# Performance work log

Measured on AMD Instinct MI355X. Metric: run time of the kernel, lower is better.

## Reference

```python
import jax, jax.numpy as jnp
import numpy as np

# KernelConv config (pinned by hard-coded views in the source)
KS = [1, 3, 5, 7]          # sorted kernel sizes
KTOT = sum(KS)             # 16
KMAX = KS[-1]              # 7
COLOR = 4                  # packed Bayer channels
RGB = 3
H = W = 48                 # hard-coded in source view


def setup_inputs() -> dict:
    key = jax.random.key(0)
    k1, k2, k3 = jax.random.split(key, 3)
    B, N = 4, 8
    frames = jax.random.normal(k1, (B, N, COLOR, H, W), dtype=jnp.float32)
    # core channels = N * 2*KTOT * COLOR * RGB = 8 * 32 * 12 = 3072
    core = jax.random.normal(k2, (B, N * 2 * KTOT * COLOR * RGB, H, W), dtype=jnp.float32)
    kernel_weight = jax.random.uniform(k3, (B, N, len(KS), RGB, H, W), dtype=jnp.float32)
    return {"frames": frames, "core": core, "kernel_weight": kernel_weight}


def _kernel_conv(frames, core, kernel_weight):
    B, N, color, h, w = frames.shape
    # --- _sep_conv_core: separable 1D cores -> 2D per-pixel cores (outer product) ---
    c = core.reshape(B, N, 2 * KTOT, color, RGB, h, w)
    c1, c2 = c[:, :, :KTOT], c[:, :, KTOT:]
    cores = {}
    cur = 0
    for K in KS:
        t1 = c1[:, :, cur:cur + K]          # [B,N,K,color,3,h,w]
        t2 = c2[:, :, cur:cur + K]
        # outer product over the two kernel axes (torch einsum ijklcnop,ijlmcnop->ijkmcnop)
        cores[K] = jnp.einsum('bnkcthw,bnlcthw->bnklcthw', t1, t2)  # [B,N,K,K,color,3,h,w]
        cur += K
    # --- pad all kernels to KMAX and stack (reversed kernel order, as in source) ---
    padded = []
    for K in KS[::-1]:
        p = (KMAX - K) // 2
        padded.append(jnp.pad(cores[K], ((0, 0), (0, 0), (p, p), (p, p), (0, 0), (0, 0), (0, 0), (0, 0))))
    pk = jnp.stack(padded, axis=2)                              # [B,N,S,KMAX,KMAX,color,3,h,w]
    pk = pk.reshape(B, N, len(KS), KMAX * KMAX * color, RGB, h, w)
    # weighted fusion across kernel scales
    wk = jnp.mean(pk * kernel_weight[:, :, :, None], axis=2)    # [B,N,KMAX^2*color,3,h,w]
    # --- img_stack: KMAX^2 shifted views of the padded frames ---
    r = KMAX // 2
    fpad = jnp.pad(frames, ((0, 0), (0, 0), (0, 0), (r, r), (r, r)))
    shifts = [fpad[..., i:i + h, j:j + w] for i in range(KMAX) for j in range(KMAX)]
    img_stack = jnp.stack(shifts, axis=2)                       # [B,N,KMAX^2,color,h,w]
    # --- per-pixel conv: sum over kernel taps and color for each RGB output ---
    wk_r = wk.reshape(B, N, KMAX * KMAX, color, RGB, h, w)
    pred_img_i = jnp.einsum('bnkcthw,bnkchw->bnthw', wk_r, img_stack)  # [B,N,3,h,w]
    pred_img = jnp.mean(pred_img_i, axis=1)                            # [B,3,h,w]
    return pred_img_i, pred_img


def reference(frames, core, kernel_weight):
    return _kernel_conv(frames, core, kernel_weight)
```

## Files before the change

### kernel.cpp

```cpp
#include <hip/hip_runtime.h>

#define HH 48
#define WW 48
#define HW 2304
#define NB 8
#define CB 4
#define TB 3


__global__ __launch_bounds__(256) void kconv_part(
    const float* __restrict__ frames,
    const float* __restrict__ core,
    const float* __restrict__ kw,
    float* __restrict__ part)
{
    const int tid = blockIdx.x * blockDim.x + threadIdx.x;
    const int pix = tid % HW;
    int rem = tid / HW;
    const int t = rem % TB; rem /= TB;
    const int c = rem % CB; rem /= CB;
    const int n = rem % NB;
    const int b = rem / NB;
    const int x = pix % WW;
    const int y = pix / WW;

    const float* kwp = kw + ((size_t)(b * NB + n) * 12 + t) * HW + pix;
    const float kw0 = kwp[0];
    const float kw1 = kwp[(size_t)3 * HW];
    const float kw2 = kwp[(size_t)6 * HW];
    const float kw3 = kwp[(size_t)9 * HW];

    const float* cp = core + ((size_t)b * 3072 + (size_t)((n * 32) * CB + c) * 3 + t) * HW + pix;
    float a[16], bv[16];
    #pragma unroll
    for (int q = 0; q < 16; ++q) {
        a[q]  = cp[(size_t)(q * 12) * HW];
        bv[q] = cp[(size_t)((q + 16) * 12) * HW];
    }

    const float* fb = frames + ((size_t)(b * NB + n) * CB + c) * HW;

    float r7 = 0.f, r5 = 0.f, r3 = 0.f, r1 = 0.f;
    #pragma unroll
    for (int i = 0; i < 7; ++i) {
        const int yy = y + i - 3;
        const bool yok = (yy >= 0) & (yy < HH);
        float fp[7];
        #pragma unroll
        for (int j = 0; j < 7; ++j) {
            const int xx = x + j - 3;
            const bool ok = yok & (xx >= 0) & (xx < WW);
            fp[j] = ok ? fb[yy * WW + xx] : 0.f;
        }
        float in7 = 0.f;
        #pragma unroll
        for (int j = 0; j < 7; ++j) in7 = fmaf(bv[9 + j], fp[j], in7);
        r7 = fmaf(a[9 + i], in7, r7);
        if (i >= 1 && i <= 5) {
            float in5 = 0.f;
            #pragma unroll
            for (int j = 0; j < 5; ++j) in5 = fmaf(bv[4 + j], fp[1 + j], in5);
            r5 = fmaf(a[4 + i - 1], in5, r5);
        }
        if (i >= 2 && i <= 4) {
            float in3 = 0.f;
            #pragma unroll
            for (int j = 0; j < 3; ++j) in3 = fmaf(bv[1 + j], fp[2 + j], in3);
            r3 = fmaf(a[1 + i - 2], in3, r3);
        }
        if (i == 3) r1 = a[0] * bv[0] * fp[3];
    }

    part[tid] = fmaf(kw0, r7, fmaf(kw1, r5, fmaf(kw2, r3, kw3 * r1)));
}

__global__ __launch_bounds__(256) void reduce_c(
    const float* __restrict__ part, float* __restrict__ out)
{
    const int tid = blockIdx.x * blockDim.x + threadIdx.x;
    const int pix3 = tid % (TB * HW);
    const int bn = tid / (TB * HW);
    const float* p = part + (size_t)bn * CB * TB * HW + pix3;
    const float s = p[0] + p[(size_t)TB * HW] + p[(size_t)2 * TB * HW] + p[(size_t)3 * TB * HW];
    out[tid] = 0.25f * s;
}

__global__ __launch_bounds__(256) void mean_kernel(
    const float* __restrict__ pii, float* __restrict__ pm)
{
    const int tid = blockIdx.x * blockDim.x + threadIdx.x;
    if (tid >= 4 * TB * HW) return;
    const int pix3 = tid % (TB * HW);
    const int b = tid / (TB * HW);
    float s = 0.f;
    #pragma unroll
    for (int n = 0; n < NB; ++n)
        s += pii[(size_t)((b * NB + n) * TB) * HW + pix3];
    pm[tid] = s * 0.125f;
}

__global__ __launch_bounds__(256) void kconv_kernel(
    const float* __restrict__ frames, const float* __restrict__ core,
    const float* __restrict__ kw, float* __restrict__ out)
{
    const int tid = blockIdx.x * blockDim.x + threadIdx.x;
    const int x = tid % WW;
    const int y = (tid / WW) % HH;
    const int n = (tid / HW) % NB;
    const int b = tid / (HW * NB);
    const int pix = y * WW + x;

    float kwv[4][3];
    {
        const float* kwp = kw + (size_t)((b * NB + n) * 12) * HW + pix;
        #pragma unroll
        for (int s = 0; s < 4; ++s)
            #pragma unroll
            for (int t = 0; t < TB; ++t)
                kwv[s][t] = kwp[(size_t)(s * 3 + t) * HW];
    }
    float acc[TB] = {0.f, 0.f, 0.f};
    const float* fbase = frames + (size_t)((b * NB + n) * CB) * HW;
    const float* cbase = core + (size_t)b * 3072 * HW + pix;
    for (int c = 0; c < CB; ++c) {
        float fpv[49];
        #pragma unroll
        for (int i = 0; i < 7; ++i) {
            const int yy = y + i - 3;
            #pragma unroll
            for (int j = 0; j < 7; ++j) {
                const int xx = x + j - 3;
                const bool ok = (yy >= 0) & (yy < HH) & (xx >= 0) & (xx < WW);
                fpv[i * 7 + j] = ok ? fbase[(size_t)c * HW + yy * WW + xx] : 0.f;
            }
        }
        #pragma unroll
        for (int t = 0; t < TB; ++t) {
            float a[16], bv[16];
            const float* cp = cbase + (size_t)(((n * 32) * CB + c) * 3 + t) * HW;
            #pragma unroll
            for (int q = 0; q < 16; ++q) {
                a[q]  = cp[(size_t)(q * 12) * HW];
                bv[q] = cp[(size_t)((q + 16) * 12) * HW];
            }
            float tot = 0.f;
            {
                float r = 0.f;
                #pragma unroll
                for (int i = 0; i < 7; ++i) {
                    float inner = 0.f;
                    #pragma unroll
                    for (int j = 0; j < 7; ++j) inner = fmaf(bv[9 + j], fpv[i * 7 + j], inner);
                    r = fmaf(a[9 + i], inner, r);
                }
                tot = fmaf(kwv[0][t], r, tot);
            }
            {
                float r = 0.f;
                #pragma unroll
                for (int i = 0; i < 5; ++i) {
                    float inner = 0.f;
                    #pragma unroll
                    for (int j = 0; j < 5; ++j) inner = fmaf(bv[4 + j], fpv[(1 + i) * 7 + 1 + j], inner);
                    r = fmaf(a[4 + i], inner, r);
                }
                tot = fmaf(kwv[1][t], r, tot);
            }
            {
                float r = 0.f;
                #pragma unroll
                for (int i = 0; i < 3; ++i) {
                    float inner = 0.f;
                    #pragma unroll
                    for (int j = 0; j < 3; ++j) inner = fmaf(bv[1 + j], fpv[(2 + i) * 7 + 2 + j], inner);
                    r = fmaf(a[1 + i], inner, r);
                }
                tot = fmaf(kwv[2][t], r, tot);
            }
            tot = fmaf(kwv[3][t], a[0] * bv[0] * fpv[3 * 7 + 3], tot);
            acc[t] += 0.25f * tot;
        }
    }
    float* op = out + (size_t)((b * NB + n) * TB) * HW + pix;
    op[0] = acc[0]; op[HW] = acc[1]; op[2 * HW] = acc[2];
}

extern "C" void kernel_launch(void* const* d_in, const int* in_sizes, int n_in,
                              void* d_out, int out_size, void* d_ws, size_t ws_size,
                              hipStream_t stream) {
    const float* frames = (const float*)d_in[0];
    const float* core   = (const float*)d_in[1];
    const float* kw     = (const float*)d_in[2];
    float* out = (float*)d_out;
    float* pm  = out + 4 * NB * TB * HW;

    const size_t part_elems = (size_t)4 * NB * CB * TB * HW;
    if (ws_size >= part_elems * sizeof(float)) {
        float* part = (float*)d_ws;
        kconv_part<<<(int)(part_elems / 256), 256, 0, stream>>>(frames, core, kw, part);
        reduce_c<<<(4 * NB * TB * HW) / 256, 256, 0, stream>>>(part, out);
    } else {
        kconv_kernel<<<(4 * NB * HW) / 256, 256, 0, stream>>>(frames, core, kw, out);
    }
    mean_kernel<<<(4 * TB * HW + 255) / 256, 256, 0, stream>>>(out, pm);
}
```

Baseline: 30.68 us.

## Fuse channel reduction and batch mean into one finish kernel, clamp frame loads

Merges the color-channel reduction and the mean-over-frames kernels into a single finish kernel, so one launch and one round trip of the per-frame output through global memory are removed. The conv kernel now clamps frame indices and loads unconditionally before masking, which avoids divergent predicated loads. It also moves the kernel_weight loads after the compute loop and sets a minimum-occupancy hint of 6 blocks per CU. The finish kernel launches far fewer threads (one per b,t,pixel, each looping over 8 frames), so it exposes less parallelism.

```diff
diff --git a/kernel.cpp b/kernel.cpp
--- a/kernel.cpp
+++ b/kernel.cpp
@@ -8,7 +8,7 @@
 #define TB 3
 
 
-__global__ __launch_bounds__(256) void kconv_part(
+__global__ __launch_bounds__(256, 6) void kconv_part(
     const float* __restrict__ frames,
     const float* __restrict__ core,
     const float* __restrict__ kw,
@@ -24,79 +24,79 @@
     const int x = pix % WW;
     const int y = pix / WW;
 
+    const float* cp = core + ((size_t)b * 3072 + (size_t)((n * 32) * CB + c) * 3 + t) * HW + pix;
+    float a[16], bv[16];
+    #pragma unroll
+    for (int q = 0; q < 16; ++q) {
+        a[q]  = cp[(size_t)(q * 12) * HW];
+        bv[q] = cp[(size_t)((q + 16) * 12) * HW];
+    }
+
+    const float* fb = frames + ((size_t)(b * NB + n) * CB + c) * HW;
+
+    float r7 = 0.f, r5 = 0.f, r3 = 0.f, r1 = 0.f;
+    #pragma unroll
+    for (int i = 0; i < 7; ++i) {
+        const int yy = y + i - 3;
+        const bool yok = (yy >= 0) & (yy < HH);
+        const int yyc = min(max(yy, 0), HH - 1);
+        const float* frow = fb + yyc * WW;
+        float fp[7];
+        #pragma unroll
+        for (int j = 0; j < 7; ++j) {
+            const int xx = x + j - 3;
+            const bool ok = yok & (xx >= 0) & (xx < WW);
+            const int xxc = min(max(xx, 0), WW - 1);
+            const float v = frow[xxc];
+            fp[j] = ok ? v : 0.f;
+        }
+        float in7 = 0.f;
+        #pragma unroll
+        for (int j = 0; j < 7; ++j) in7 = fmaf(bv[9 + j], fp[j], in7);
+        r7 = fmaf(a[9 + i], in7, r7);
+        if (i >= 1 && i <= 5) {
+            float in5 = 0.f;
+            #pragma unroll
+            for (int j = 0; j < 5; ++j) in5 = fmaf(bv[4 + j], fp[1 + j], in5);
+            r5 = fmaf(a[4 + i - 1], in5, r5);
+        }
+        if (i >= 2 && i <= 4) {
+            float in3 = 0.f;
+            #pragma unroll
+            for (int j = 0; j < 3; ++j) in3 = fmaf(bv[1 + j], fp[2 + j], in3);
+            r3 = fmaf(a[1 + i - 2], in3, r3);
+        }
+        if (i == 3) r1 = a[0] * bv[0] * fp[3];
+    }
+
     const float* kwp = kw + ((size_t)(b * NB + n) * 12 + t) * HW + pix;
     const float kw0 = kwp[0];
     const float kw1 = kwp[(size_t)3 * HW];
     const float kw2 = kwp[(size_t)6 * HW];
     const float kw3 = kwp[(size_t)9 * HW];
 
-    const float* cp = core + ((size_t)b * 3072 + (size_t)((n * 32) * CB + c) * 3 + t) * HW + pix;
-    float a[16], bv[16];
-    #pragma unroll
-    for (int q = 0; q < 16; ++q) {
-        a[q]  = cp[(size_t)(q * 12) * HW];
-        bv[q] = cp[(size_t)((q + 16) * 12) * HW];
-    }
-
-    const float* fb = frames + ((size_t)(b * NB + n) * CB + c) * HW;
-
-    float r7 = 0.f, r5 = 0.f, r3 = 0.f, r1 = 0.f;
-    #pragma unroll
-    for (int i = 0; i < 7; ++i) {
-        const int yy = y + i - 3;
-        const bool yok = (yy >= 0) & (yy < HH);
-        float fp[7];
-        #pragma unroll
-        for (int j = 0; j < 7; ++j) {
-            const int xx = x + j - 3;
-            const bool ok = yok & (xx >= 0) & (xx < WW);
-            fp[j] = ok ? fb[yy * WW + xx] : 0.f;
-        }
-        float in7 = 0.f;
-        #pragma unroll
-        for (int j = 0; j < 7; ++j) in7 = fmaf(bv[9 + j], fp[j], in7);
-        r7 = fmaf(a[9 + i], in7, r7);
-        if (i >= 1 && i <= 5) {
-            float in5 = 0.f;
-            #pragma unroll
-            for (int j = 0; j < 5; ++j) in5 = fmaf(bv[4 + j], fp[1 + j], in5);
-            r5 = fmaf(a[4 + i - 1], in5, r5);
-        }
-        if (i >= 2 && i <= 4) {
-            float in3 = 0.f;
-            #pragma unroll
-            for (int j = 0; j < 3; ++j) in3 = fmaf(bv[1 + j], fp[2 + j], in3);
-            r3 = fmaf(a[1 + i - 2], in3, r3);
-        }
-        if (i == 3) r1 = a[0] * bv[0] * fp[3];
-    }
-
     part[tid] = fmaf(kw0, r7, fmaf(kw1, r5, fmaf(kw2, r3, kw3 * r1)));
 }
 
-__global__ __launch_bounds__(256) void reduce_c(
-    const float* __restrict__ part, float* __restrict__ out)
-{
-    const int tid = blockIdx.x * blockDim.x + threadIdx.x;
-    const int pix3 = tid % (TB * HW);
-    const int bn = tid / (TB * HW);
-    const float* p = part + (size_t)bn * CB * TB * HW + pix3;
-    const float s = p[0] + p[(size_t)TB * HW] + p[(size_t)2 * TB * HW] + p[(size_t)3 * TB * HW];
-    out[tid] = 0.25f * s;
-}
-
-__global__ __launch_bounds__(256) void mean_kernel(
-    const float* __restrict__ pii, float* __restrict__ pm)
+__global__ __launch_bounds__(256) void finish(
+    const float* __restrict__ part, float* __restrict__ out, float* __restrict__ pm)
 {
     const int tid = blockIdx.x * blockDim.x + threadIdx.x;
     if (tid >= 4 * TB * HW) return;
-    const int pix3 = tid % (TB * HW);
-    const int b = tid / (TB * HW);
-    float s = 0.f;
-    #pragma unroll
-    for (int n = 0; n < NB; ++n)
-        s += pii[(size_t)((b * NB + n) * TB) * HW + pix3];
-    pm[tid] = s * 0.125f;
+    const int pix = tid % HW;
+    const int t = (tid / HW) % TB;
+    const int b = tid / (HW * TB);
+
+    float m = 0.f;
+    #pragma unroll
+    for (int n = 0; n < NB; ++n) {
+        const float* p = part + ((size_t)((b * NB + n) * CB) * TB + t) * HW + pix;
+        float s = p[0] + p[(size_t)TB * HW] + p[(size_t)2 * TB * HW] + p[(size_t)3 * TB * HW];
+        s *= 0.25f;
+        out[((size_t)(b * NB + n) * TB + t) * HW + pix] = s;
+        m += s;
+    }
+    pm[((size_t)b * TB + t) * HW + pix] = m * 0.125f;
 }
 
 __global__ __launch_bounds__(256) void kconv_kernel(
@@ -185,6 +185,20 @@
     op[0] = acc[0]; op[HW] = acc[1]; op[2 * HW] = acc[2];
 }
 
+__global__ __launch_bounds__(256) void mean_fb(
+    const float* __restrict__ pii, float* __restrict__ pm)
+{
+    const int tid = blockIdx.x * blockDim.x + threadIdx.x;
+    if (tid >= 4 * TB * HW) return;
+    const int pix3 = tid % (TB * HW);
+    const int b = tid / (TB * HW);
+    float s = 0.f;
+    #pragma unroll
+    for (int n = 0; n < NB; ++n)
+        s += pii[(size_t)((b * NB + n) * TB) * HW + pix3];
+    pm[tid] = s * 0.125f;
+}
+
 extern "C" void kernel_launch(void* const* d_in, const int* in_sizes, int n_in,
                               void* d_out, int out_size, void* d_ws, size_t ws_size,
                               hipStream_t stream) {
@@ -198,9 +212,9 @@
     if (ws_size >= part_elems * sizeof(float)) {
         float* part = (float*)d_ws;
         kconv_part<<<(int)(part_elems / 256), 256, 0, stream>>>(frames, core, kw, part);
-        reduce_c<<<(4 * NB * TB * HW) / 256, 256, 0, stream>>>(part, out);
+        finish<<<(4 * TB * HW + 255) / 256, 256, 0, stream>>>(part, out, pm);
     } else {
         kconv_kernel<<<(4 * NB * HW) / 256, 256, 0, stream>>>(frames, core, kw, out);
-    }
-    mean_kernel<<<(4 * TB * HW + 255) / 256, 256, 0, stream>>>(out, pm);
-}
+        mean_fb<<<(4 * TB * HW + 255) / 256, 256, 0, stream>>>(out, pm);
+    }
+}
```

Measured after the change: 68.45 us. +123.1%, slower.
